# Optimization experiments

Measured on AMD Instinct MI355X. Metric: run time of the kernel, lower is better.

Reference implementation:

```python
import jax, jax.numpy as jnp
import numpy as np
import math

D_MODEL = 2048
R = 512
N_HEADS = 16
D_K = R // N_HEADS  # 32
B = 2
S = 2048


def _xavier(key, out_dim, in_dim):
    limit = math.sqrt(6.0 / (in_dim + out_dim))
    return jax.random.uniform(key, (out_dim, in_dim), jnp.float32, -limit, limit)


def setup_inputs() -> dict:
    key = jax.random.key(0)
    ks = jax.random.split(key, 6)
    x = jax.random.normal(ks[0], (B, S, D_MODEL), dtype=jnp.float32)
    mask = jnp.ones((B, 1, 1, S), dtype=jnp.int32)
    # torch nn.Linear weights have shape (out, in)
    Wq = _xavier(ks[1], R, D_MODEL)
    Wk = _xavier(ks[2], R, D_MODEL)
    Wv = _xavier(ks[3], R, D_MODEL)
    Wo = _xavier(ks[4], D_MODEL, R)
    bq = jnp.zeros((R,), jnp.float32)
    bk = jnp.zeros((R,), jnp.float32)
    bv = jnp.zeros((R,), jnp.float32)
    bo = jnp.zeros((D_MODEL,), jnp.float32)
    return {"x": x, "Wq": Wq, "bq": bq, "Wk": Wk, "bk": bk,
            "Wv": Wv, "bv": bv, "Wo": Wo, "bo": bo, "mask": mask}


def reference(x, Wq, bq, Wk, bk, Wv, bv, Wo, bo, mask):
    b, s, _ = x.shape
    scale = math.sqrt(D_K)
    # projections: (B,S,d_model) @ (d_model,r) -> (B,S,r)
    Q = x @ Wq.T + bq
    K = x @ Wk.T + bk
    V = x @ Wv.T + bv
    # (B,S,r) -> (B,H,S,d_k)
    Q = Q.reshape(b, s, N_HEADS, D_K).transpose(0, 2, 1, 3)
    K = K.reshape(b, s, N_HEADS, D_K).transpose(0, 2, 1, 3)
    V = V.reshape(b, s, N_HEADS, D_K).transpose(0, 2, 1, 3)
    # scores: (B,H,Sq,Sk)
    scores = jnp.einsum('bhqd,bhkd->bhqk', Q, K) / scale
    scores = jnp.where(mask == 0, -jnp.inf, scores)
    attn = jax.nn.softmax(scores, axis=-1)  # dropout p=0 (eval)
    out = jnp.einsum('bhqk,bhkd->bhqd', attn, V)
    out = out.transpose(0, 2, 1, 3).reshape(b, s, R)
    return out @ Wo.T + bo
```

## Files before the change

### kernel.cpp

```cpp
#include <hip/hip_runtime.h>
#include <hip/hip_bf16.h>
#include <math.h>

typedef __attribute__((ext_vector_type(8))) short bf16x8;
typedef __attribute__((ext_vector_type(4))) float f32x4;

#define D_MODEL 2048
#define R_DIM 512
#define N_HEADS 16
#define D_K 32
#define B_SZ 2
#define SEQ 2048
#define M_ROWS (B_SZ * SEQ)
#define N_QKV 1536
#define QSCALE 0.2550627231338903f

__device__ __forceinline__ void dma16(const void* g, void* l)
{
    __builtin_amdgcn_global_load_lds(
        (const __attribute__((address_space(1))) void*)g,
        (__attribute__((address_space(3))) void*)l, 16, 0, 0);
}

__device__ __forceinline__ unsigned cvt_pk_bf16(float lo, float hi)
{
    unsigned r;
    asm("v_cvt_pk_bf16_f32 %0, %1, %2" : "=v"(r) : "v"(lo), "v"(hi));
    return r;
}

__global__ __launch_bounds__(256) void cvt_inputs(
    const float* __restrict__ x,  __hip_bfloat16* __restrict__ xb,
    const float* __restrict__ Wq, const float* __restrict__ Wk,
    const float* __restrict__ Wv, const float* __restrict__ Wo,
    __hip_bfloat16* __restrict__ Wqkvb, __hip_bfloat16* __restrict__ Wob,
    const float* __restrict__ bq, const float* __restrict__ bk,
    const float* __restrict__ bv, float* __restrict__ bias_qkv,
    const int* __restrict__ mask, float* __restrict__ mbias)
{
    const int by = blockIdx.y;
    const int tid = blockIdx.x * blockDim.x + threadIdx.x;
    const int nthr = gridDim.x * blockDim.x;
    if (by == 5) {
        for (int i = tid; i < N_QKV; i += nthr) {
            float v = (i < 512) ? bq[i] * QSCALE
                    : (i < 1024) ? bk[i - 512] : bv[i - 1024];
            bias_qkv[i] = v;
        }
        for (int i = tid; i < B_SZ * SEQ; i += nthr)
            mbias[i] = mask[i] ? 0.0f : -1e30f;
        return;
    }
    const float* src; __hip_bfloat16* dst; float sc = 1.0f; int n;
    switch (by) {
      case 0: src = Wq; dst = Wqkvb; sc = QSCALE; n = R_DIM * D_MODEL; break;
      case 1: src = Wk; dst = Wqkvb + (size_t)R_DIM * D_MODEL; n = R_DIM * D_MODEL; break;
      case 2: src = Wv; dst = Wqkvb + (size_t)2 * R_DIM * D_MODEL; n = R_DIM * D_MODEL; break;
      case 3: src = Wo; dst = Wob; n = D_MODEL * R_DIM; break;
      default: src = x;  dst = xb;  n = M_ROWS * D_MODEL; break;
    }
    const float4* s4 = (const float4*)src;
    ushort4* d4 = (ushort4*)dst;
    const int n4 = n >> 2;
    const int step = nthr * 4;
    for (int i0 = tid; i0 < n4; i0 += step) {
        float4 f0 = s4[i0];
        float4 f1 = s4[i0 + nthr];
        float4 f2 = s4[i0 + 2 * nthr];
        float4 f3 = s4[i0 + 3 * nthr];
        union { ushort4 u; __hip_bfloat16 h[4]; } r0, r1, r2, r3;
        r0.h[0] = __float2bfloat16(f0.x * sc); r0.h[1] = __float2bfloat16(f0.y * sc);
        r0.h[2] = __float2bfloat16(f0.z * sc); r0.h[3] = __float2bfloat16(f0.w * sc);
        r1.h[0] = __float2bfloat16(f1.x * sc); r1.h[1] = __float2bfloat16(f1.y * sc);
        r1.h[2] = __float2bfloat16(f1.z * sc); r1.h[3] = __float2bfloat16(f1.w * sc);
        r2.h[0] = __float2bfloat16(f2.x * sc); r2.h[1] = __float2bfloat16(f2.y * sc);
        r2.h[2] = __float2bfloat16(f2.z * sc); r2.h[3] = __float2bfloat16(f2.w * sc);
        r3.h[0] = __float2bfloat16(f3.x * sc); r3.h[1] = __float2bfloat16(f3.y * sc);
        r3.h[2] = __float2bfloat16(f3.z * sc); r3.h[3] = __float2bfloat16(f3.w * sc);
        d4[i0]            = r0.u;
        d4[i0 + nthr]     = r1.u;
        d4[i0 + 2 * nthr] = r2.u;
        d4[i0 + 3 * nthr] = r3.u;
    }
}

template<bool OUT_BF16>
__global__ __launch_bounds__(256, 4) void gemm_dma(
    const __hip_bfloat16* __restrict__ A,
    const __hip_bfloat16* __restrict__ W,
    const float* __restrict__ bias,
    void* __restrict__ Cv,
    int N, int K)
{
    __shared__ __hip_bfloat16 As[128 * 64];
    __shared__ __hip_bfloat16 Bs[64 * 64];

    const int tid = threadIdx.x, lane = tid & 63, w = tid >> 6;
    const int l15 = lane & 15, q = lane >> 4;
    const int bm = blockIdx.y * 128, bn = blockIdx.x * 64;
    const int m_off = (w & 1) * 64, n_off = (w >> 1) * 32;

    const int lrow = lane >> 3;
    const int lc   = (lane & 7) ^ lrow;

    f32x4 acc[4][2] = {};

    for (int kt = 0; kt < K; kt += 64) {
        if (kt) __syncthreads();
        #pragma unroll
        for (int j = 0; j < 4; j++) {
            int row = (w * 4 + j) * 8 + lrow;
            dma16(&A[(size_t)(bm + row) * K + kt + lc * 8], &As[(w * 4 + j) * 512]);
        }
        #pragma unroll
        for (int j = 0; j < 2; j++) {
            int row = (w * 2 + j) * 8 + lrow;
            dma16(&W[(size_t)(bn + row) * K + kt + lc * 8], &Bs[(w * 2 + j) * 512]);
        }
        __syncthreads();

        #pragma unroll
        for (int ks = 0; ks < 2; ks++) {
            bf16x8 af[4], bf[2];
            #pragma unroll
            for (int t = 0; t < 4; t++) {
                int row = m_off + t * 16 + l15;
                af[t] = *(const bf16x8*)&As[row * 64 + (((ks * 4 + q) ^ (l15 & 7)) * 8)];
            }
            #pragma unroll
            for (int u = 0; u < 2; u++) {
                int row = n_off + u * 16 + l15;
                bf[u] = *(const bf16x8*)&Bs[row * 64 + (((ks * 4 + q) ^ (l15 & 7)) * 8)];
            }
            #pragma unroll
            for (int mt = 0; mt < 4; mt++)
                #pragma unroll
                for (int nt = 0; nt < 2; nt++)
                    acc[mt][nt] = __builtin_amdgcn_mfma_f32_16x16x32_bf16(
                        af[mt], bf[nt], acc[mt][nt], 0, 0, 0);
        }
    }

    #pragma unroll
    for (int mt = 0; mt < 4; mt++) {
        #pragma unroll
        for (int nt = 0; nt < 2; nt++) {
            int gm = bm + m_off + mt * 16 + q * 4;
            int gn = bn + n_off + nt * 16 + l15;
            float bv = bias[gn];
            #pragma unroll
            for (int r = 0; r < 4; r++) {
                float v = acc[mt][nt][r] + bv;
                if (OUT_BF16)
                    ((__hip_bfloat16*)Cv)[(size_t)(gm + r) * N + gn] = __float2bfloat16(v);
                else
                    ((float*)Cv)[(size_t)(gm + r) * N + gn] = v;
            }
        }
    }
}

__global__ __launch_bounds__(256, 4) void flash_attn8(
    const __hip_bfloat16* __restrict__ QKV,
    const float* __restrict__ mbias,
    __hip_bfloat16* __restrict__ O)
{
    __shared__ __hip_bfloat16 Ks[2][64 * 40];
    __shared__ __hip_bfloat16 Vt[2][32 * 72];

    const int tid = threadIdx.x, lane = tid & 63, w = tid >> 6;
    const int l15 = lane & 15, qg = lane >> 4;

    const int nwg = (int)gridDim.x;
    const int swz = ((int)blockIdx.x & 7) * (nwg >> 3) + ((int)blockIdx.x >> 3);
    const int qt = swz & 15;
    const int h  = (swz >> 4) & 15;
    const int b  = swz >> 8;
    const int q0 = qt * 128;

    const bf16x8 qa0 = *(const bf16x8*)
        &QKV[(size_t)(b * SEQ + q0 + w * 32 + l15) * N_QKV + h * D_K + qg * 8];
    const bf16x8 qa1 = *(const bf16x8*)
        &QKV[(size_t)(b * SEQ + q0 + w * 32 + 16 + l15) * N_QKV + h * D_K + qg * 8];

    const int kv_k = tid >> 2, d0_k = (tid & 3) * 8;
    const int kv_v = tid & 63, d0_v = (tid >> 6) * 8;
    const int scol_v = (kv_v & 32) + ((kv_v >> 2) & 3) * 8
                     + ((kv_v >> 4) & 1) * 4 + (kv_v & 3);

    const __hip_bfloat16* Kp = QKV + (size_t)b * SEQ * N_QKV + R_DIM + h * D_K;
    const __hip_bfloat16* Vp = QKV + (size_t)b * SEQ * N_QKV + 2 * R_DIM + h * D_K;
    const float* mb_base = mbias + b * SEQ;

    f32x4 oaccA[2] = {};
    f32x4 oaccB[2] = {};
    float rsum0 = 0.f, rsum1 = 0.f;

    uint4 kregA, kregB, vregA, vregB;

    kregA = *(const uint4*)&Kp[(size_t)kv_k * N_QKV + d0_k];
    vregA = *(const uint4*)&Vp[(size_t)kv_v * N_QKV + d0_v];

#define FA_EXP(SC, MB, PA, U0, U1, RS)                                          \
    {                                                                           \
        float p0 = __builtin_amdgcn_exp2f(SC[0] + MB.x);                        \
        float p1 = __builtin_amdgcn_exp2f(SC[1] + MB.y);                        \
        float p2 = __builtin_amdgcn_exp2f(SC[2] + MB.z);                        \
        float p3 = __builtin_amdgcn_exp2f(SC[3] + MB.w);                        \
        RS += (p0 + p1) + (p2 + p3);                                            \
        PA.u[U0] = cvt_pk_bf16(p0, p1);                                         \
        PA.u[U1] = cvt_pk_bf16(p2, p3);                                         \
    }

#define FA_ITER(KT, BUF, KREG, VREG, KREGN, VREGN)                              \
    {                                                                           \
                  \
        *(uint4*)&Ks[BUF][kv_k * 40 + d0_k] = KREG;                             \
        { union { uint4 u; __hip_bfloat16 hv[8]; } vv; vv.u = VREG;             \
          _Pragma("unroll")                                                     \
          for (int j = 0; j < 8; j++)                                           \
              Vt[BUF][(d0_v + j) * 72 + scol_v] = vv.hv[j]; }                   \
        __syncthreads();                                                        \
         \
        float4 mb0 = *(const float4*)&mb_base[(KT) +  0 + qg * 4];              \
        float4 mb1 = *(const float4*)&mb_base[(KT) + 16 + qg * 4];              \
        float4 mb2 = *(const float4*)&mb_base[(KT) + 32 + qg * 4];              \
        float4 mb3 = *(const float4*)&mb_base[(KT) + 48 + qg * 4];              \
                 \
        if ((KT) + 64 < SEQ) {                                                  \
            KREGN = *(const uint4*)&Kp[(size_t)((KT) + 64 + kv_k) * N_QKV + d0_k]; \
            VREGN = *(const uint4*)&Vp[(size_t)((KT) + 64 + kv_v) * N_QKV + d0_v]; \
        }                                                                       \
                               \
        f32x4 a0, a1, a2, a3, b0, b1, b2, b3;                                   \
        __builtin_amdgcn_s_setprio(1);                                          \
        { bf16x8 kb = *(const bf16x8*)&Ks[BUF][( 0 + l15) * 40 + qg * 8];       \
          f32x4 z = {};                                                         \
          a0 = __builtin_amdgcn_mfma_f32_16x16x32_bf16(kb, qa0, z, 0, 0, 0);    \
          b0 = __builtin_amdgcn_mfma_f32_16x16x32_bf16(kb, qa1, z, 0, 0, 0); }  \
        { bf16x8 kb = *(const bf16x8*)&Ks[BUF][(16 + l15) * 40 + qg * 8];       \
          f32x4 z = {};                                                         \
          a1 = __builtin_amdgcn_mfma_f32_16x16x32_bf16(kb, qa0, z, 0, 0, 0);    \
          b1 = __builtin_amdgcn_mfma_f32_16x16x32_bf16(kb, qa1, z, 0, 0, 0); }  \
        { bf16x8 kb = *(const bf16x8*)&Ks[BUF][(32 + l15) * 40 + qg * 8];       \
          f32x4 z = {};                                                         \
          a2 = __builtin_amdgcn_mfma_f32_16x16x32_bf16(kb, qa0, z, 0, 0, 0);    \
          b2 = __builtin_amdgcn_mfma_f32_16x16x32_bf16(kb, qa1, z, 0, 0, 0); }  \
        { bf16x8 kb = *(const bf16x8*)&Ks[BUF][(48 + l15) * 40 + qg * 8];       \
          f32x4 z = {};                                                         \
          a3 = __builtin_amdgcn_mfma_f32_16x16x32_bf16(kb, qa0, z, 0, 0, 0);    \
          b3 = __builtin_amdgcn_mfma_f32_16x16x32_bf16(kb, qa1, z, 0, 0, 0); }  \
        __builtin_amdgcn_s_setprio(0);                                          \
              \
        union { unsigned u[4]; bf16x8 v; } paA0, paA1, paB0, paB1;              \
        FA_EXP(a0, mb0, paA0, 0, 1, rsum0)                                      \
        FA_EXP(a1, mb1, paA0, 2, 3, rsum0)                                      \
        FA_EXP(a2, mb2, paA1, 0, 1, rsum0)                                      \
        FA_EXP(a3, mb3, paA1, 2, 3, rsum0)                                      \
        FA_EXP(b0, mb0, paB0, 0, 1, rsum1)                                      \
        FA_EXP(b1, mb1, paB0, 2, 3, rsum1)                                      \
        FA_EXP(b2, mb2, paB1, 0, 1, rsum1)                                      \
        FA_EXP(b3, mb3, paB1, 2, 3, rsum1)                                      \
                      \
        __builtin_amdgcn_s_setprio(1);                                          \
        _Pragma("unroll")                                                       \
        for (int dt = 0; dt < 2; dt++) {                                        \
            const __hip_bfloat16* vrow = &Vt[BUF][(dt * 16 + l15) * 72];        \
            bf16x8 vb0 = *(const bf16x8*)&vrow[qg * 8];                         \
            bf16x8 vb1 = *(const bf16x8*)&vrow[32 + qg * 8];                    \
            oaccA[dt] = __builtin_amdgcn_mfma_f32_16x16x32_bf16(paA0.v, vb0, oaccA[dt], 0, 0, 0); \
            oaccA[dt] = __builtin_amdgcn_mfma_f32_16x16x32_bf16(paA1.v, vb1, oaccA[dt], 0, 0, 0); \
            oaccB[dt] = __builtin_amdgcn_mfma_f32_16x16x32_bf16(paB0.v, vb0, oaccB[dt], 0, 0, 0); \
            oaccB[dt] = __builtin_amdgcn_mfma_f32_16x16x32_bf16(paB1.v, vb1, oaccB[dt], 0, 0, 0); \
        }                                                                       \
        __builtin_amdgcn_s_setprio(0);                                          \
    }

    for (int kt = 0; kt < SEQ; kt += 128) {
        FA_ITER(kt,      0, kregA, vregA, kregB, vregB)
        FA_ITER(kt + 64, 1, kregB, vregB, kregA, vregA)
    }
#undef FA_ITER
#undef FA_EXP

    float s0 = rsum0, s1 = rsum1;
    s0 += __shfl_xor(s0, 16, 64);
    s0 += __shfl_xor(s0, 32, 64);
    s1 += __shfl_xor(s1, 16, 64);
    s1 += __shfl_xor(s1, 32, 64);

    #pragma unroll
    for (int r = 0; r < 4; r++) {
        float invA = 1.0f / __shfl(s0, qg * 4 + r, 64);
        float invB = 1.0f / __shfl(s1, qg * 4 + r, 64);
        int rowA = q0 + w * 32 + qg * 4 + r;
        int rowB = rowA + 16;
        #pragma unroll
        for (int dt = 0; dt < 2; dt++) {
            O[(size_t)(b * SEQ + rowA) * R_DIM + h * D_K + dt * 16 + l15] =
                __float2bfloat16(oaccA[dt][r] * invA);
            O[(size_t)(b * SEQ + rowB) * R_DIM + h * D_K + dt * 16 + l15] =
                __float2bfloat16(oaccB[dt][r] * invB);
        }
    }
}

extern "C" void kernel_launch(void* const* d_in, const int* in_sizes, int n_in,
                              void* d_out, int out_size, void* d_ws, size_t ws_size,
                              hipStream_t stream)
{
    const float* x  = (const float*)d_in[0];
    const float* Wq = (const float*)d_in[1];
    const float* bq = (const float*)d_in[2];
    const float* Wk = (const float*)d_in[3];
    const float* bk = (const float*)d_in[4];
    const float* Wv = (const float*)d_in[5];
    const float* bv = (const float*)d_in[6];
    const float* Wo = (const float*)d_in[7];
    const float* bo = (const float*)d_in[8];
    const int* mask = (const int*)d_in[9];
    float* out = (float*)d_out;

    char* p = (char*)d_ws;
    __hip_bfloat16* xb     = (__hip_bfloat16*)p;
    __hip_bfloat16* AO     = xb;
    __hip_bfloat16* Wqkvb  = (__hip_bfloat16*)(p + (16u << 20));
    __hip_bfloat16* Wob    = (__hip_bfloat16*)(p + (22u << 20));
    float*          biasq  = (float*)(p + (24u << 20));
    float*          mbias  = (float*)(p + (24u << 20) + 8192);
    __hip_bfloat16* QKVb   = (__hip_bfloat16*)(p + (25u << 20));

    dim3 blk(256);
    hipLaunchKernelGGL(cvt_inputs, dim3(256, 6), blk, 0, stream,
                       x, xb, Wq, Wk, Wv, Wo, Wqkvb, Wob, bq, bk, bv, biasq, mask, mbias);
    hipLaunchKernelGGL((gemm_dma<true>), dim3(N_QKV / 64, M_ROWS / 128), blk, 0, stream,
                       xb, Wqkvb, biasq, QKVb, N_QKV, D_MODEL);
    hipLaunchKernelGGL(flash_attn8, dim3(B_SZ * N_HEADS * (SEQ / 128)), blk, 0, stream,
                       QKVb, mbias, AO);
    hipLaunchKernelGGL((gemm_dma<false>), dim3(D_MODEL / 64, M_ROWS / 128), blk, 0, stream,
                       AO, Wob, bo, out, D_MODEL, R_DIM);
}
```

Measured before the change: 187.0 us.

## Double attention query tile to 256 rows per workgroup for K/V reuse

```diff
diff --git a/kernel.cpp b/kernel.cpp
--- a/kernel.cpp
+++ b/kernel.cpp
@@ -160,7 +160,7 @@
     }
 }
 
-__global__ __launch_bounds__(256, 4) void flash_attn8(
+__global__ __launch_bounds__(256, 1) void flash_attn10(
     const __hip_bfloat16* __restrict__ QKV,
     const float* __restrict__ mbias,
     __hip_bfloat16* __restrict__ O)
@@ -173,15 +173,16 @@
 
     const int nwg = (int)gridDim.x;
     const int swz = ((int)blockIdx.x & 7) * (nwg >> 3) + ((int)blockIdx.x >> 3);
-    const int qt = swz & 15;
-    const int h  = (swz >> 4) & 15;
-    const int b  = swz >> 8;
-    const int q0 = qt * 128;
-
-    const bf16x8 qa0 = *(const bf16x8*)
-        &QKV[(size_t)(b * SEQ + q0 + w * 32 + l15) * N_QKV + h * D_K + qg * 8];
-    const bf16x8 qa1 = *(const bf16x8*)
-        &QKV[(size_t)(b * SEQ + q0 + w * 32 + 16 + l15) * N_QKV + h * D_K + qg * 8];
+    const int qt = swz & 7;
+    const int h  = (swz >> 3) & 15;
+    const int b  = swz >> 7;
+    const int q0 = qt * 256;
+
+    bf16x8 qa[4];
+    #pragma unroll
+    for (int c = 0; c < 4; c++)
+        qa[c] = *(const bf16x8*)
+            &QKV[(size_t)(b * SEQ + q0 + w * 64 + c * 16 + l15) * N_QKV + h * D_K + qg * 8];
 
     const int kv_k = tid >> 2, d0_k = (tid & 3) * 8;
     const int kv_v = tid & 63, d0_v = (tid >> 6) * 8;
@@ -192,9 +193,8 @@
     const __hip_bfloat16* Vp = QKV + (size_t)b * SEQ * N_QKV + 2 * R_DIM + h * D_K;
     const float* mb_base = mbias + b * SEQ;
 
-    f32x4 oaccA[2] = {};
-    f32x4 oaccB[2] = {};
-    float rsum0 = 0.f, rsum1 = 0.f;
+    f32x4 oacc[4][2] = {};
+    float rsum[4] = {0.f, 0.f, 0.f, 0.f};
 
     uint4 kregA, kregB, vregA, vregB;
 
@@ -221,7 +221,7 @@
           for (int j = 0; j < 8; j++)                                           \
               Vt[BUF][(d0_v + j) * 72 + scol_v] = vv.hv[j]; }                   \
         __syncthreads();                                                        \
-         \
+                                      \
         float4 mb0 = *(const float4*)&mb_base[(KT) +  0 + qg * 4];              \
         float4 mb1 = *(const float4*)&mb_base[(KT) + 16 + qg * 4];              \
         float4 mb2 = *(const float4*)&mb_base[(KT) + 32 + qg * 4];              \
@@ -231,47 +231,43 @@
             KREGN = *(const uint4*)&Kp[(size_t)((KT) + 64 + kv_k) * N_QKV + d0_k]; \
             VREGN = *(const uint4*)&Vp[(size_t)((KT) + 64 + kv_v) * N_QKV + d0_v]; \
         }                                                                       \
-                               \
-        f32x4 a0, a1, a2, a3, b0, b1, b2, b3;                                   \
+              \
+        f32x4 sc[4][4];                                                         \
         __builtin_amdgcn_s_setprio(1);                                          \
-        { bf16x8 kb = *(const bf16x8*)&Ks[BUF][( 0 + l15) * 40 + qg * 8];       \
-          f32x4 z = {};                                                         \
-          a0 = __builtin_amdgcn_mfma_f32_16x16x32_bf16(kb, qa0, z, 0, 0, 0);    \
-          b0 = __builtin_amdgcn_mfma_f32_16x16x32_bf16(kb, qa1, z, 0, 0, 0); }  \
-        { bf16x8 kb = *(const bf16x8*)&Ks[BUF][(16 + l15) * 40 + qg * 8];       \
-          f32x4 z = {};                                                         \
-          a1 = __builtin_amdgcn_mfma_f32_16x16x32_bf16(kb, qa0, z, 0, 0, 0);    \
-          b1 = __builtin_amdgcn_mfma_f32_16x16x32_bf16(kb, qa1, z, 0, 0, 0); }  \
-        { bf16x8 kb = *(const bf16x8*)&Ks[BUF][(32 + l15) * 40 + qg * 8];       \
-          f32x4 z = {};                                                         \
-          a2 = __builtin_amdgcn_mfma_f32_16x16x32_bf16(kb, qa0, z, 0, 0, 0);    \
-          b2 = __builtin_amdgcn_mfma_f32_16x16x32_bf16(kb, qa1, z, 0, 0, 0); }  \
-        { bf16x8 kb = *(const bf16x8*)&Ks[BUF][(48 + l15) * 40 + qg * 8];       \
-          f32x4 z = {};                                                         \
-          a3 = __builtin_amdgcn_mfma_f32_16x16x32_bf16(kb, qa0, z, 0, 0, 0);    \
-          b3 = __builtin_amdgcn_mfma_f32_16x16x32_bf16(kb, qa1, z, 0, 0, 0); }  \
+        _Pragma("unroll")                                                       \
+        for (int nt = 0; nt < 4; nt++) {                                        \
+            bf16x8 kb = *(const bf16x8*)&Ks[BUF][(nt * 16 + l15) * 40 + qg * 8];\
+            _Pragma("unroll")                                                   \
+            for (int c = 0; c < 4; c++) {                                       \
+                f32x4 z = {};                                                   \
+                sc[nt][c] = __builtin_amdgcn_mfma_f32_16x16x32_bf16(            \
+                    kb, qa[c], z, 0, 0, 0);                                     \
+            }                                                                   \
+        }                                                                       \
         __builtin_amdgcn_s_setprio(0);                                          \
-              \
-        union { unsigned u[4]; bf16x8 v; } paA0, paA1, paB0, paB1;              \
-        FA_EXP(a0, mb0, paA0, 0, 1, rsum0)                                      \
-        FA_EXP(a1, mb1, paA0, 2, 3, rsum0)                                      \
-        FA_EXP(a2, mb2, paA1, 0, 1, rsum0)                                      \
-        FA_EXP(a3, mb3, paA1, 2, 3, rsum0)                                      \
-        FA_EXP(b0, mb0, paB0, 0, 1, rsum1)                                      \
-        FA_EXP(b1, mb1, paB0, 2, 3, rsum1)                                      \
-        FA_EXP(b2, mb2, paB1, 0, 1, rsum1)                                      \
-        FA_EXP(b3, mb3, paB1, 2, 3, rsum1)                                      \
-                      \
+                \
+        union { unsigned u[4]; bf16x8 v; } pa0[4], pa1[4];                      \
+        _Pragma("unroll")                                                       \
+        for (int c = 0; c < 4; c++) {                                           \
+            FA_EXP(sc[0][c], mb0, pa0[c], 0, 1, rsum[c])                        \
+            FA_EXP(sc[1][c], mb1, pa0[c], 2, 3, rsum[c])                        \
+            FA_EXP(sc[2][c], mb2, pa1[c], 0, 1, rsum[c])                        \
+            FA_EXP(sc[3][c], mb3, pa1[c], 2, 3, rsum[c])                        \
+        }                                                                       \
+                           \
         __builtin_amdgcn_s_setprio(1);                                          \
         _Pragma("unroll")                                                       \
         for (int dt = 0; dt < 2; dt++) {                                        \
             const __hip_bfloat16* vrow = &Vt[BUF][(dt * 16 + l15) * 72];        \
             bf16x8 vb0 = *(const bf16x8*)&vrow[qg * 8];                         \
             bf16x8 vb1 = *(const bf16x8*)&vrow[32 + qg * 8];                    \
-            oaccA[dt] = __builtin_amdgcn_mfma_f32_16x16x32_bf16(paA0.v, vb0, oaccA[dt], 0, 0, 0); \
-            oaccA[dt] = __builtin_amdgcn_mfma_f32_16x16x32_bf16(paA1.v, vb1, oaccA[dt], 0, 0, 0); \
-            oaccB[dt] = __builtin_amdgcn_mfma_f32_16x16x32_bf16(paB0.v, vb0, oaccB[dt], 0, 0, 0); \
-            oaccB[dt] = __builtin_amdgcn_mfma_f32_16x16x32_bf16(paB1.v, vb1, oaccB[dt], 0, 0, 0); \
+            _Pragma("unroll")                                                   \
+            for (int c = 0; c < 4; c++) {                                       \
+                oacc[c][dt] = __builtin_amdgcn_mfma_f32_16x16x32_bf16(          \
+                    pa0[c].v, vb0, oacc[c][dt], 0, 0, 0);                       \
+                oacc[c][dt] = __builtin_amdgcn_mfma_f32_16x16x32_bf16(          \
+                    pa1[c].v, vb1, oacc[c][dt], 0, 0, 0);                       \
+            }                                                                   \
         }                                                                       \
         __builtin_amdgcn_s_setprio(0);                                          \
     }
@@ -283,24 +279,20 @@
 #undef FA_ITER
 #undef FA_EXP
 
-    float s0 = rsum0, s1 = rsum1;
-    s0 += __shfl_xor(s0, 16, 64);
-    s0 += __shfl_xor(s0, 32, 64);
-    s1 += __shfl_xor(s1, 16, 64);
-    s1 += __shfl_xor(s1, 32, 64);
-
     #pragma unroll
-    for (int r = 0; r < 4; r++) {
-        float invA = 1.0f / __shfl(s0, qg * 4 + r, 64);
-        float invB = 1.0f / __shfl(s1, qg * 4 + r, 64);
-        int rowA = q0 + w * 32 + qg * 4 + r;
-        int rowB = rowA + 16;
-        #pragma unroll
-        for (int dt = 0; dt < 2; dt++) {
-            O[(size_t)(b * SEQ + rowA) * R_DIM + h * D_K + dt * 16 + l15] =
-                __float2bfloat16(oaccA[dt][r] * invA);
-            O[(size_t)(b * SEQ + rowB) * R_DIM + h * D_K + dt * 16 + l15] =
-                __float2bfloat16(oaccB[dt][r] * invB);
+    for (int c = 0; c < 4; c++) {
+        float s = rsum[c];
+        s += __shfl_xor(s, 16, 64);
+        s += __shfl_xor(s, 32, 64);
+        #pragma unroll
+        for (int r = 0; r < 4; r++) {
+            float inv = 1.0f / __shfl(s, qg * 4 + r, 64);
+            int row = q0 + w * 64 + c * 16 + qg * 4 + r;
+            #pragma unroll
+            for (int dt = 0; dt < 2; dt++) {
+                O[(size_t)(b * SEQ + row) * R_DIM + h * D_K + dt * 16 + l15] =
+                    __float2bfloat16(oacc[c][dt][r] * inv);
+            }
         }
     }
 }
@@ -335,7 +327,7 @@
                        x, xb, Wq, Wk, Wv, Wo, Wqkvb, Wob, bq, bk, bv, biasq, mask, mbias);
     hipLaunchKernelGGL((gemm_dma<true>), dim3(N_QKV / 64, M_ROWS / 128), blk, 0, stream,
                        xb, Wqkvb, biasq, QKVb, N_QKV, D_MODEL);
-    hipLaunchKernelGGL(flash_attn8, dim3(B_SZ * N_HEADS * (SEQ / 128)), blk, 0, stream,
+    hipLaunchKernelGGL(flash_attn10, dim3(B_SZ * N_HEADS * (SEQ / 256)), blk, 0, stream,
                        QKVb, mbias, AO);
     hipLaunchKernelGGL((gemm_dma<false>), dim3(D_MODEL / 64, M_ROWS / 128), blk, 0, stream,
                        AO, Wob, bo, out, D_MODEL, R_DIM);
```

Result: slower. 195.4 us (+4.5%).
